# Performance work log

Measured on AMD Instinct MI355X. Metric: run time of the kernel, lower is better.

The kernel has to match this reference:

```python
import jax, jax.numpy as jnp
import numpy as np

B, N, E, DIN, DH = 32, 2000, 64000, 128, 128


def setup_inputs() -> dict:
    key = jax.random.key(0)
    ks = jax.random.split(key, 8)
    gene_emb = jax.random.normal(ks[0], (B, N, DIN), dtype=jnp.float32)
    edge_src = jax.random.randint(ks[1], (E,), 0, N, dtype=jnp.int32)
    edge_dst = jax.random.randint(ks[2], (E,), 0, N, dtype=jnp.int32)
    s1 = 1.0 / np.sqrt(DIN)
    s2 = 1.0 / np.sqrt(DH)
    W1 = jax.random.normal(ks[3], (DIN, DH), dtype=jnp.float32) * s1
    b1 = jnp.zeros((DH,), dtype=jnp.float32)
    W2 = jax.random.normal(ks[4], (DH, DH), dtype=jnp.float32) * s2
    b2 = jnp.zeros((DH,), dtype=jnp.float32)
    return {"gene_emb": gene_emb, "edge_src": edge_src, "edge_dst": edge_dst,
            "W1": W1, "b1": b1, "W2": W2, "b2": b2, "pathway_idx": 0}


def _gcn_conv(x, src, dst, norm_e, self_norm, W, b):
    # x: [B, N, Din] -> [B, N, Dout]; PyG GCNConv: linear first, then normalized aggregation
    h = jnp.einsum('bnd,de->bne', x, W)
    msgs = h[:, src, :] * norm_e[None, :, None]          # [B, E, Dout] gather
    agg = jax.vmap(lambda m: jax.ops.segment_sum(m, dst, num_segments=h.shape[1]))(msgs)
    # self-loop contribution (A+I): norm = dinv[i]^2
    return agg + h * self_norm[None, :, None] + b


def reference(gene_emb, edge_src, edge_dst, W1, b1, W2, b2, pathway_idx):
    n = gene_emb.shape[1]
    # symmetric GCN normalization with self loops: deg[i] = in_degree + 1
    deg = jnp.zeros((n,), dtype=gene_emb.dtype).at[edge_dst].add(1.0) + 1.0
    dinv = jax.lax.rsqrt(deg)
    norm_e = dinv[edge_src] * dinv[edge_dst]
    self_norm = dinv * dinv
    x = jax.nn.relu(_gcn_conv(gene_emb, edge_src, edge_dst, norm_e, self_norm, W1, b1))
    x = _gcn_conv(x, edge_src, edge_dst, norm_e, self_norm, W2, b2)
    # global_mean_pool over each graph copy (all graphs have n nodes)
    return jnp.mean(x, axis=1)  # [B, DH]
```

## Files before the change

kernel.cpp:

```cpp
#include <hip/hip_runtime.h>

namespace {
constexpr int NB = 32;
constexpr int NN = 2000;
constexpr int NE = 64000;
constexpr int ND = 128;
constexpr int TR = 16;
constexpr int NCHUNK = NN / TR;
constexpr int NXCD = 8;
constexpr int BPB = 2;
constexpr int PAIRS_PER_XCD = NB / (NXCD * BPB);
constexpr int NPAIR = NB / BPB;
constexpr int GRID_FUSED = NPAIR * NCHUNK;
constexpr int SL = 80;

constexpr int CVT_BLOCKS  = 1000;
constexpr int W_BLOCKS    = 8;
constexpr int EDGE_BLOCKS = 250;

constexpr size_t OFF_CNT    = 0;
constexpr size_t OFF_CNT2   = 8192;
constexpr size_t OFF_WSUM   = 16384;
constexpr size_t MEMSET_BYTES = 24576;
constexpr size_t OFF_SLOT2  = 24576;
constexpr size_t OFF_WF     = OFF_SLOT2 + (size_t)NN * SL * 8;
constexpr size_t OFF_YP     = OFF_WF + 32768;
constexpr size_t OFF_XBF    = OFF_YP + (size_t)NB * NCHUNK * ND * 4;

typedef __attribute__((ext_vector_type(8))) short bf16x8;
typedef __attribute__((ext_vector_type(4))) float f32x4;

__device__ __forceinline__ ushort f32_to_bf16(float f) {
    uint u = __float_as_uint(f);
    u += 0x7fffu + ((u >> 16) & 1u);
    return (ushort)(u >> 16);
}
__device__ __forceinline__ uint pack_bf16x2(float lo, float hi) {
    return (uint)f32_to_bf16(lo) | ((uint)f32_to_bf16(hi) << 16);
}
}

__global__ void k_prep1(const float* __restrict__ X, ushort* __restrict__ xbf,
                        const float* __restrict__ W1, uint* __restrict__ wf,
                        const int* __restrict__ dst, int* __restrict__ cnt) {
    const int blk = blockIdx.x;
    if (blk < CVT_BLOCKS) {
        const float4* __restrict__ X4 = (const float4*)X;
        ushort4* __restrict__ O4 = (ushort4*)xbf;
        const int base = blk * 2048 + (int)threadIdx.x;
        #pragma unroll
        for (int k = 0; k < 8; k++) {
            int i = base + k * 256;
            float4 v = X4[i];
            ushort4 o;
            o.x = f32_to_bf16(v.x);
            o.y = f32_to_bf16(v.y);
            o.z = f32_to_bf16(v.z);
            o.w = f32_to_bf16(v.w);
            O4[i] = o;
        }
    } else if (blk < CVT_BLOCKS + W_BLOCKS) {
        int g = (blk - CVT_BLOCKS) * 256 + threadIdx.x;
        int lane = g & 63, f = g >> 6;
        int nt = f >> 2, kc = f & 3;
        int col = nt * 16 + (lane & 15);
        int k0  = kc * 32 + (lane >> 4) * 8;
        uint4 o;
        o.x = pack_bf16x2(W1[(k0 + 0) * ND + col], W1[(k0 + 1) * ND + col]);
        o.y = pack_bf16x2(W1[(k0 + 2) * ND + col], W1[(k0 + 3) * ND + col]);
        o.z = pack_bf16x2(W1[(k0 + 4) * ND + col], W1[(k0 + 5) * ND + col]);
        o.w = pack_bf16x2(W1[(k0 + 6) * ND + col], W1[(k0 + 7) * ND + col]);
        ((uint4*)wf)[g] = o;
    } else {
        int e = (blk - CVT_BLOCKS - W_BLOCKS) * 256 + threadIdx.x;
        atomicAdd(&cnt[dst[e]], 1);
    }
}

__global__ void k_prep2(const int* __restrict__ src, const int* __restrict__ dst,
                        const int* __restrict__ cnt, int* __restrict__ cnt2,
                        float* __restrict__ wsum, int2* __restrict__ slot2) {
    int e = blockIdx.x * 256 + threadIdx.x;
    int s = src[e], d = dst[e];
    float w = rsqrtf((float)(cnt[s] + 1)) * rsqrtf((float)(cnt[d] + 1));
    int p = atomicAdd(&cnt2[d], 1);
    if (p < SL) slot2[(size_t)d * SL + p] = make_int2(s, __float_as_int(w));
    atomicAdd(&wsum[s], w);
}

__global__ __launch_bounds__(256, 4) void k_fused(const ushort* __restrict__ xbf,
                                                  const int* __restrict__ cnt,
                                                  const int2* __restrict__ slot2,
                                                  const float* __restrict__ wsum,
                                                  const uint* __restrict__ wfrag,
                                                  const float* __restrict__ b1,
                                                  float* __restrict__ ypart) {
    __shared__ __align__(16) uint AsU[2][TR * 68];
    __shared__ int2  sE[TR][SL];
    __shared__ float sDinv[TR];
    __shared__ float sWn[TR];
    __shared__ int   sCnt[TR];
    const int tid = threadIdx.x;

    const int L     = blockIdx.x;
    const int xcd   = L & (NXCD - 1);
    const int sl    = L >> 3;
    const int pair  = sl / NCHUNK;
    const int chunk = sl - pair * NCHUNK;
    const int b0    = xcd * (BPB * PAIRS_PER_XCD) + pair * BPB;
    const int n0    = chunk * TR;

    if (tid < TR) {
        int n = n0 + tid;
        int cr = cnt[n];
        float d = rsqrtf((float)(cr + 1));
        sCnt[tid]  = min(cr, SL);
        sDinv[tid] = d;
        sWn[tid]   = wsum[n] + d * d;
    }
    __syncthreads();

    const int wv = tid >> 6, ln = tid & 63;
    const int p = ln >> 5, col = ln & 31;
    const uint2* __restrict__ X0 = (const uint2*)(xbf + (size_t)b0 * NN * ND);
    const uint2* __restrict__ X1 = X0 + (size_t)NN * ND / 4;

    bf16x8 wfv[2][4];
    const bf16x8* Wf8 = (const bf16x8*)wfrag;
    #pragma unroll
    for (int nt2 = 0; nt2 < 2; nt2++)
        #pragma unroll
        for (int kc = 0; kc < 4; kc++)
            wfv[nt2][kc] = Wf8[(((2 * wv + nt2) * 4 + kc) * 64) + ln];

    #pragma unroll
    for (int ii = 0; ii < 4; ii++) {
        int j = wv * 4 + ii;
        int c = sCnt[j];
        const int2* sp = slot2 + (size_t)(n0 + j) * SL;
        for (int base = 0; base < c; base += 64)
            if (base + ln < c) sE[j][base + ln] = sp[base + ln];
    }

    #pragma unroll 1
    for (int ii = 0; ii < 4; ii++) {
        const int j = wv * 4 + ii;
        const int n = n0 + j;
        const int c = sCnt[j];
        float4 a  = {0.f, 0.f, 0.f, 0.f}, ab = a;
        float4 g  = a, gb = a;
        {
            uint2 q = X0[(size_t)p * (NN * ND / 4) + n * 32 + col];
            float sn = sDinv[j] * sDinv[j];
            float w0 = p ? 0.f : sn;
            float w1 = p ? sn : 0.f;
            float f0 = __uint_as_float(q.x << 16);
            float f1 = __uint_as_float(q.x & 0xffff0000u);
            float f2 = __uint_as_float(q.y << 16);
            float f3 = __uint_as_float(q.y & 0xffff0000u);
            a.x = w0 * f0; a.y = w0 * f1; a.z = w0 * f2; a.w = w0 * f3;
            g.x = w1 * f0; g.y = w1 * f1; g.z = w1 * f2; g.w = w1 * f3;
        }
        int e = 0;
        for (; e + 8 <= c; e += 8) {
            int sidx[4]; float w[4]; uint2 q0[4], q1[4];
            #pragma unroll
            for (int q = 0; q < 4; q++) {
                int2 ed = sE[j][e + 2 * q + p];
                sidx[q] = ed.x; w[q] = __int_as_float(ed.y);
            }
            #pragma unroll
            for (int q = 0; q < 4; q++) {
                int off = sidx[q] * 32 + col;
                q0[q] = X0[off];
                q1[q] = X1[off];
            }
            #pragma unroll
            for (int q = 0; q < 4; q++) {
                float f0 = __uint_as_float(q0[q].x << 16);
                float f1 = __uint_as_float(q0[q].x & 0xffff0000u);
                float f2 = __uint_as_float(q0[q].y << 16);
                float f3 = __uint_as_float(q0[q].y & 0xffff0000u);
                float h0 = __uint_as_float(q1[q].x << 16);
                float h1 = __uint_as_float(q1[q].x & 0xffff0000u);
                float h2 = __uint_as_float(q1[q].y << 16);
                float h3 = __uint_as_float(q1[q].y & 0xffff0000u);
                if (q & 1) {
                    ab.x = fmaf(w[q], f0, ab.x); ab.y = fmaf(w[q], f1, ab.y);
                    ab.z = fmaf(w[q], f2, ab.z); ab.w = fmaf(w[q], f3, ab.w);
                    gb.x = fmaf(w[q], h0, gb.x); gb.y = fmaf(w[q], h1, gb.y);
                    gb.z = fmaf(w[q], h2, gb.z); gb.w = fmaf(w[q], h3, gb.w);
                } else {
                    a.x = fmaf(w[q], f0, a.x); a.y = fmaf(w[q], f1, a.y);
                    a.z = fmaf(w[q], f2, a.z); a.w = fmaf(w[q], f3, a.w);
                    g.x = fmaf(w[q], h0, g.x); g.y = fmaf(w[q], h1, g.y);
                    g.z = fmaf(w[q], h2, g.z); g.w = fmaf(w[q], h3, g.w);
                }
            }
        }
        for (; e < c; e += 2) {
            int ee = e + p;
            int eidx = (ee < c) ? ee : e;
            int2 ed = sE[j][eidx];
            float w = (ee < c) ? __int_as_float(ed.y) : 0.f;
            int off = ed.x * 32 + col;
            uint2 u0 = X0[off], u1 = X1[off];
            a.x = fmaf(w, __uint_as_float(u0.x << 16), a.x);
            a.y = fmaf(w, __uint_as_float(u0.x & 0xffff0000u), a.y);
            a.z = fmaf(w, __uint_as_float(u0.y << 16), a.z);
            a.w = fmaf(w, __uint_as_float(u0.y & 0xffff0000u), a.w);
            g.x = fmaf(w, __uint_as_float(u1.x << 16), g.x);
            g.y = fmaf(w, __uint_as_float(u1.x & 0xffff0000u), g.y);
            g.z = fmaf(w, __uint_as_float(u1.y << 16), g.z);
            g.w = fmaf(w, __uint_as_float(u1.y & 0xffff0000u), g.w);
        }
        a.x += ab.x; a.y += ab.y; a.z += ab.z; a.w += ab.w;
        g.x += gb.x; g.y += gb.y; g.z += gb.z; g.w += gb.w;
        a.x += __shfl_xor(a.x, 32); a.y += __shfl_xor(a.y, 32);
        a.z += __shfl_xor(a.z, 32); a.w += __shfl_xor(a.w, 32);
        g.x += __shfl_xor(g.x, 32); g.y += __shfl_xor(g.y, 32);
        g.z += __shfl_xor(g.z, 32); g.w += __shfl_xor(g.w, 32);
        float4 av;
        av.x = p ? g.x : a.x; av.y = p ? g.y : a.y;
        av.z = p ? g.z : a.z; av.w = p ? g.w : a.w;
        AsU[p][j * 68 + 2 * col]     = pack_bf16x2(av.x, av.y);
        AsU[p][j * 68 + 2 * col + 1] = pack_bf16x2(av.z, av.w);
    }
    __syncthreads();

    const int lane15 = ln & 15, quad = ln >> 4;
    f32x4 zero4 = {0.f, 0.f, 0.f, 0.f};
    f32x4 acc[2][2];
    acc[0][0] = zero4; acc[0][1] = zero4; acc[1][0] = zero4; acc[1][1] = zero4;

    const bf16x8* A0 = (const bf16x8*)AsU[0];
    const bf16x8* A1 = (const bf16x8*)AsU[1];
    #pragma unroll
    for (int kc = 0; kc < 4; kc++) {
        bf16x8 af0 = A0[lane15 * 17 + kc * 4 + quad];
        bf16x8 af1 = A1[lane15 * 17 + kc * 4 + quad];
        #pragma unroll
        for (int nt2 = 0; nt2 < 2; nt2++) {
            acc[0][nt2] = __builtin_amdgcn_mfma_f32_16x16x32_bf16(
                af0, wfv[nt2][kc], acc[0][nt2], 0, 0, 0);
            acc[1][nt2] = __builtin_amdgcn_mfma_f32_16x16x32_bf16(
                af1, wfv[nt2][kc], acc[1][nt2], 0, 0, 0);
        }
    }

    #pragma unroll
    for (int nt2 = 0; nt2 < 2; nt2++) {
        int cg = (2 * wv + nt2) * 16 + lane15;
        float bias = b1[cg];
        #pragma unroll
        for (int b = 0; b < 2; b++) {
            float part = 0.f;
            #pragma unroll
            for (int r = 0; r < 4; r++)
                part = fmaf(sWn[quad * 4 + r], fmaxf(acc[b][nt2][r] + bias, 0.f), part);
            part += __shfl_xor(part, 16);
            part += __shfl_xor(part, 32);
            if (quad == 0)
                ypart[((size_t)(b0 + b) * NCHUNK + chunk) * ND + cg] = part;
        }
    }
}

__global__ __launch_bounds__(128) void k_out(const float* __restrict__ ypart,
                                             const float* __restrict__ W2,
                                             const float* __restrict__ b2,
                                             float* __restrict__ out) {
    __shared__ float ys[128];
    const int b = blockIdx.x;
    const int d = threadIdx.x;
    float s = 0.f;
    for (int c = 0; c < NCHUNK; c++)
        s += ypart[((size_t)b * NCHUNK + c) * ND + d];
    ys[d] = s * (1.f / (float)NN);
    __syncthreads();
    float acc = b2[d];
    #pragma unroll 8
    for (int k = 0; k < 128; k++)
        acc = fmaf(ys[k], W2[k * ND + d], acc);
    out[b * ND + d] = acc;
}

extern "C" void kernel_launch(void* const* d_in, const int* in_sizes, int n_in,
                              void* d_out, int out_size, void* d_ws, size_t ws_size,
                              hipStream_t stream) {
    (void)in_sizes; (void)n_in; (void)out_size; (void)ws_size;
    const float* X   = (const float*)d_in[0];
    const int*   src = (const int*)d_in[1];
    const int*   dst = (const int*)d_in[2];
    const float* W1  = (const float*)d_in[3];
    const float* b1  = (const float*)d_in[4];
    const float* W2  = (const float*)d_in[5];
    const float* b2  = (const float*)d_in[6];
    float* out = (float*)d_out;

    char* ws = (char*)d_ws;
    int*    cnt   = (int*)   (ws + OFF_CNT);
    int*    cnt2  = (int*)   (ws + OFF_CNT2);
    float*  wsum  = (float*) (ws + OFF_WSUM);
    int2*   slot2 = (int2*)  (ws + OFF_SLOT2);
    uint*   wfb   = (uint*)  (ws + OFF_WF);
    float*  ypart = (float*) (ws + OFF_YP);
    ushort* xbf   = (ushort*)(ws + OFF_XBF);

    (void)hipMemsetAsync(ws, 0, MEMSET_BYTES, stream);
    k_prep1<<<CVT_BLOCKS + W_BLOCKS + EDGE_BLOCKS, 256, 0, stream>>>(
        X, xbf, W1, wfb, dst, cnt);
    k_prep2<<<EDGE_BLOCKS, 256, 0, stream>>>(src, dst, cnt, cnt2, wsum, slot2);
    k_fused<<<GRID_FUSED, 256, 0, stream>>>(xbf, cnt, slot2, wsum, wfb, b1, ypart);
    k_out<<<NB, 128, 0, stream>>>(ypart, W2, b2, out);
}
```

Baseline: 169.0 us.

## Merge all stages into one cooperative persistent kernel with grid syncs

```diff
diff --git a/kernel.cpp b/kernel.cpp
--- a/kernel.cpp
+++ b/kernel.cpp
@@ -1,4 +1,7 @@
 #include <hip/hip_runtime.h>
+#include <hip/hip_cooperative_groups.h>
+
+namespace cg = cooperative_groups;
 
 namespace {
 constexpr int NB = 32;
@@ -10,10 +13,10 @@
 constexpr int NXCD = 8;
 constexpr int BPB = 2;
 constexpr int PAIRS_PER_XCD = NB / (NXCD * BPB);
-constexpr int NPAIR = NB / BPB;
-constexpr int GRID_FUSED = NPAIR * NCHUNK;
+constexpr int GRID_FUSED = (NB / BPB) * NCHUNK;
 constexpr int SL = 80;
 
+constexpr int GRID_MEGA   = 1000;
 constexpr int CVT_BLOCKS  = 1000;
 constexpr int W_BLOCKS    = 8;
 constexpr int EDGE_BLOCKS = 250;
@@ -38,6 +41,274 @@
 __device__ __forceinline__ uint pack_bf16x2(float lo, float hi) {
     return (uint)f32_to_bf16(lo) | ((uint)f32_to_bf16(hi) << 16);
 }
+
+__device__ __forceinline__ void wpack_item(const float* __restrict__ W1,
+                                           uint* __restrict__ wf, int g) {
+    int lane = g & 63, f = g >> 6;
+    int nt = f >> 2, kc = f & 3;
+    int colw = nt * 16 + (lane & 15);
+    int k0  = kc * 32 + (lane >> 4) * 8;
+    uint4 o;
+    o.x = pack_bf16x2(W1[(k0 + 0) * ND + colw], W1[(k0 + 1) * ND + colw]);
+    o.y = pack_bf16x2(W1[(k0 + 2) * ND + colw], W1[(k0 + 3) * ND + colw]);
+    o.z = pack_bf16x2(W1[(k0 + 4) * ND + colw], W1[(k0 + 5) * ND + colw]);
+    o.w = pack_bf16x2(W1[(k0 + 6) * ND + colw], W1[(k0 + 7) * ND + colw]);
+    ((uint4*)wf)[g] = o;
+}
+
+__device__ __forceinline__ void fused_tile(const ushort* __restrict__ xbf,
+                                           const int* __restrict__ cnt,
+                                           const int2* __restrict__ slot2,
+                                           const float* __restrict__ wsum,
+                                           const uint* __restrict__ wfrag,
+                                           const float* __restrict__ b1,
+                                           float* __restrict__ ypart,
+                                           int xcd, int chunk, int pair0, int npair,
+                                           int tid) {
+    __shared__ __align__(16) uint AsU[2][TR * 68];
+    __shared__ int2  sE[TR][SL];
+    __shared__ float sDinv[TR];
+    __shared__ float sWn[TR];
+    __shared__ int   sCnt[TR];
+
+    const int n0 = chunk * TR;
+    if (tid < TR) {
+        int n = n0 + tid;
+        int cr = cnt[n];
+        float d = rsqrtf((float)(cr + 1));
+        sCnt[tid]  = min(cr, SL);
+        sDinv[tid] = d;
+        sWn[tid]   = wsum[n] + d * d;
+    }
+    __syncthreads();
+
+    const int wv = tid >> 6, ln = tid & 63;
+    const int p = ln >> 5, col = ln & 31;
+
+    bf16x8 wfv[2][4];
+    const bf16x8* Wf8 = (const bf16x8*)wfrag;
+    #pragma unroll
+    for (int nt2 = 0; nt2 < 2; nt2++)
+        #pragma unroll
+        for (int kc = 0; kc < 4; kc++)
+            wfv[nt2][kc] = Wf8[(((2 * wv + nt2) * 4 + kc) * 64) + ln];
+
+    #pragma unroll
+    for (int ii = 0; ii < 4; ii++) {
+        int j = wv * 4 + ii;
+        int c = sCnt[j];
+        const int2* sp = slot2 + (size_t)(n0 + j) * SL;
+        for (int base = 0; base < c; base += 64)
+            if (base + ln < c) sE[j][base + ln] = sp[base + ln];
+    }
+
+    for (int pr = pair0; pr < pair0 + npair; ++pr) {
+        const int b0 = xcd * (BPB * PAIRS_PER_XCD) + pr * BPB;
+        const uint2* __restrict__ X0 = (const uint2*)(xbf + (size_t)b0 * NN * ND);
+        const uint2* __restrict__ X1 = X0 + (size_t)NN * ND / 4;
+
+        #pragma unroll 1
+        for (int ii = 0; ii < 4; ii++) {
+            const int j = wv * 4 + ii;
+            const int n = n0 + j;
+            const int c = sCnt[j];
+            float4 a  = {0.f, 0.f, 0.f, 0.f}, ab = a;
+            float4 g  = a, gb = a;
+            {
+                uint2 q = X0[(size_t)p * (NN * ND / 4) + n * 32 + col];
+                float sn = sDinv[j] * sDinv[j];
+                float w0 = p ? 0.f : sn;
+                float w1 = p ? sn : 0.f;
+                float f0 = __uint_as_float(q.x << 16);
+                float f1 = __uint_as_float(q.x & 0xffff0000u);
+                float f2 = __uint_as_float(q.y << 16);
+                float f3 = __uint_as_float(q.y & 0xffff0000u);
+                a.x = w0 * f0; a.y = w0 * f1; a.z = w0 * f2; a.w = w0 * f3;
+                g.x = w1 * f0; g.y = w1 * f1; g.z = w1 * f2; g.w = w1 * f3;
+            }
+            int e = 0;
+            for (; e + 8 <= c; e += 8) {
+                int sidx[4]; float w[4]; uint2 q0[4], q1[4];
+                #pragma unroll
+                for (int q = 0; q < 4; q++) {
+                    int2 ed = sE[j][e + 2 * q + p];
+                    sidx[q] = ed.x; w[q] = __int_as_float(ed.y);
+                }
+                #pragma unroll
+                for (int q = 0; q < 4; q++) {
+                    int off = sidx[q] * 32 + col;
+                    q0[q] = X0[off];
+                    q1[q] = X1[off];
+                }
+                #pragma unroll
+                for (int q = 0; q < 4; q++) {
+                    float f0 = __uint_as_float(q0[q].x << 16);
+                    float f1 = __uint_as_float(q0[q].x & 0xffff0000u);
+                    float f2 = __uint_as_float(q0[q].y << 16);
+                    float f3 = __uint_as_float(q0[q].y & 0xffff0000u);
+                    float h0 = __uint_as_float(q1[q].x << 16);
+                    float h1 = __uint_as_float(q1[q].x & 0xffff0000u);
+                    float h2 = __uint_as_float(q1[q].y << 16);
+                    float h3 = __uint_as_float(q1[q].y & 0xffff0000u);
+                    if (q & 1) {
+                        ab.x = fmaf(w[q], f0, ab.x); ab.y = fmaf(w[q], f1, ab.y);
+                        ab.z = fmaf(w[q], f2, ab.z); ab.w = fmaf(w[q], f3, ab.w);
+                        gb.x = fmaf(w[q], h0, gb.x); gb.y = fmaf(w[q], h1, gb.y);
+                        gb.z = fmaf(w[q], h2, gb.z); gb.w = fmaf(w[q], h3, gb.w);
+                    } else {
+                        a.x = fmaf(w[q], f0, a.x); a.y = fmaf(w[q], f1, a.y);
+                        a.z = fmaf(w[q], f2, a.z); a.w = fmaf(w[q], f3, a.w);
+                        g.x = fmaf(w[q], h0, g.x); g.y = fmaf(w[q], h1, g.y);
+                        g.z = fmaf(w[q], h2, g.z); g.w = fmaf(w[q], h3, g.w);
+                    }
+                }
+            }
+            for (; e < c; e += 2) {
+                int ee = e + p;
+                int eidx = (ee < c) ? ee : e;
+                int2 ed = sE[j][eidx];
+                float w = (ee < c) ? __int_as_float(ed.y) : 0.f;
+                int off = ed.x * 32 + col;
+                uint2 u0 = X0[off], u1 = X1[off];
+                a.x = fmaf(w, __uint_as_float(u0.x << 16), a.x);
+                a.y = fmaf(w, __uint_as_float(u0.x & 0xffff0000u), a.y);
+                a.z = fmaf(w, __uint_as_float(u0.y << 16), a.z);
+                a.w = fmaf(w, __uint_as_float(u0.y & 0xffff0000u), a.w);
+                g.x = fmaf(w, __uint_as_float(u1.x << 16), g.x);
+                g.y = fmaf(w, __uint_as_float(u1.x & 0xffff0000u), g.y);
+                g.z = fmaf(w, __uint_as_float(u1.y << 16), g.z);
+                g.w = fmaf(w, __uint_as_float(u1.y & 0xffff0000u), g.w);
+            }
+            a.x += ab.x; a.y += ab.y; a.z += ab.z; a.w += ab.w;
+            g.x += gb.x; g.y += gb.y; g.z += gb.z; g.w += gb.w;
+            a.x += __shfl_xor(a.x, 32); a.y += __shfl_xor(a.y, 32);
+            a.z += __shfl_xor(a.z, 32); a.w += __shfl_xor(a.w, 32);
+            g.x += __shfl_xor(g.x, 32); g.y += __shfl_xor(g.y, 32);
+            g.z += __shfl_xor(g.z, 32); g.w += __shfl_xor(g.w, 32);
+            float4 av;
+            av.x = p ? g.x : a.x; av.y = p ? g.y : a.y;
+            av.z = p ? g.z : a.z; av.w = p ? g.w : a.w;
+            AsU[p][j * 68 + 2 * col]     = pack_bf16x2(av.x, av.y);
+            AsU[p][j * 68 + 2 * col + 1] = pack_bf16x2(av.z, av.w);
+        }
+        __syncthreads();
+
+        const int lane15 = ln & 15, quad = ln >> 4;
+        f32x4 zero4 = {0.f, 0.f, 0.f, 0.f};
+        f32x4 acc[2][2];
+        acc[0][0] = zero4; acc[0][1] = zero4; acc[1][0] = zero4; acc[1][1] = zero4;
+
+        const bf16x8* A0 = (const bf16x8*)AsU[0];
+        const bf16x8* A1 = (const bf16x8*)AsU[1];
+        #pragma unroll
+        for (int kc = 0; kc < 4; kc++) {
+            bf16x8 af0 = A0[lane15 * 17 + kc * 4 + quad];
+            bf16x8 af1 = A1[lane15 * 17 + kc * 4 + quad];
+            #pragma unroll
+            for (int nt2 = 0; nt2 < 2; nt2++) {
+                acc[0][nt2] = __builtin_amdgcn_mfma_f32_16x16x32_bf16(
+                    af0, wfv[nt2][kc], acc[0][nt2], 0, 0, 0);
+                acc[1][nt2] = __builtin_amdgcn_mfma_f32_16x16x32_bf16(
+                    af1, wfv[nt2][kc], acc[1][nt2], 0, 0, 0);
+            }
+        }
+
+        #pragma unroll
+        for (int nt2 = 0; nt2 < 2; nt2++) {
+            int cg = (2 * wv + nt2) * 16 + lane15;
+            float bias = b1[cg];
+            #pragma unroll
+            for (int b = 0; b < 2; b++) {
+                float part = 0.f;
+                #pragma unroll
+                for (int r = 0; r < 4; r++)
+                    part = fmaf(sWn[quad * 4 + r], fmaxf(acc[b][nt2][r] + bias, 0.f),
+                                part);
+                part += __shfl_xor(part, 16);
+                part += __shfl_xor(part, 32);
+                if (quad == 0)
+                    ypart[((size_t)(b0 + b) * NCHUNK + chunk) * ND + cg] = part;
+            }
+        }
+        __syncthreads();
+    }
+}
+}
+
+__global__ __launch_bounds__(256, 4) void k_mega(const float* __restrict__ X,
+                                                 ushort* __restrict__ xbf,
+                                                 const float* __restrict__ W1,
+                                                 uint* __restrict__ wf,
+                                                 const int* __restrict__ src,
+                                                 const int* __restrict__ dst,
+                                                 int* __restrict__ cnt,
+                                                 int* __restrict__ cnt2,
+                                                 float* __restrict__ wsum,
+                                                 int2* __restrict__ slot2,
+                                                 const float* __restrict__ b1,
+                                                 float* __restrict__ ypart,
+                                                 const float* __restrict__ W2,
+                                                 const float* __restrict__ b2,
+                                                 float* __restrict__ out) {
+    cg::grid_group grid = cg::this_grid();
+    const int blk = blockIdx.x;
+    const int tid = threadIdx.x;
+
+    {
+        const float4* __restrict__ X4 = (const float4*)X;
+        ushort4* __restrict__ O4 = (ushort4*)xbf;
+        const int base = blk * 256 + tid;
+        #pragma unroll
+        for (int k = 0; k < 8; k++) {
+            int i = base + k * (GRID_MEGA * 256);
+            float4 v = X4[i];
+            ushort4 o;
+            o.x = f32_to_bf16(v.x);
+            o.y = f32_to_bf16(v.y);
+            o.z = f32_to_bf16(v.z);
+            o.w = f32_to_bf16(v.w);
+            O4[i] = o;
+        }
+        if (blk < EDGE_BLOCKS) {
+            int e = blk * 256 + tid;
+            atomicAdd(&cnt[dst[e]], 1);
+        } else if (blk < EDGE_BLOCKS + W_BLOCKS) {
+            wpack_item(W1, wf, (blk - EDGE_BLOCKS) * 256 + tid);
+        }
+    }
+    grid.sync();
+
+    if (blk < EDGE_BLOCKS) {
+        int e = blk * 256 + tid;
+        int s = src[e], d = dst[e];
+        float w = rsqrtf((float)(cnt[s] + 1)) * rsqrtf((float)(cnt[d] + 1));
+        int ps = atomicAdd(&cnt2[d], 1);
+        if (ps < SL) slot2[(size_t)d * SL + ps] = make_int2(s, __float_as_int(w));
+        atomicAdd(&wsum[s], w);
+    }
+    grid.sync();
+
+    fused_tile(xbf, cnt, slot2, wsum, wf, b1, ypart, blk & (NXCD - 1), blk >> 3,
+               0, PAIRS_PER_XCD, tid);
+    grid.sync();
+
+    if (blk < NB) {
+        __shared__ float ys[ND];
+        if (tid < ND) {
+            float s = 0.f;
+            for (int c = 0; c < NCHUNK; c++)
+                s += ypart[((size_t)blk * NCHUNK + c) * ND + tid];
+            ys[tid] = s * (1.f / (float)NN);
+        }
+        __syncthreads();
+        if (tid < ND) {
+            float a2 = b2[tid];
+            #pragma unroll 8
+            for (int k = 0; k < ND; k++)
+                a2 = fmaf(ys[k], W2[k * ND + tid], a2);
+            out[blk * ND + tid] = a2;
+        }
+    }
 }
 
 __global__ void k_prep1(const float* __restrict__ X, ushort* __restrict__ xbf,
@@ -60,17 +331,7 @@
             O4[i] = o;
         }
     } else if (blk < CVT_BLOCKS + W_BLOCKS) {
-        int g = (blk - CVT_BLOCKS) * 256 + threadIdx.x;
-        int lane = g & 63, f = g >> 6;
-        int nt = f >> 2, kc = f & 3;
-        int col = nt * 16 + (lane & 15);
-        int k0  = kc * 32 + (lane >> 4) * 8;
-        uint4 o;
-        o.x = pack_bf16x2(W1[(k0 + 0) * ND + col], W1[(k0 + 1) * ND + col]);
-        o.y = pack_bf16x2(W1[(k0 + 2) * ND + col], W1[(k0 + 3) * ND + col]);
-        o.z = pack_bf16x2(W1[(k0 + 4) * ND + col], W1[(k0 + 5) * ND + col]);
-        o.w = pack_bf16x2(W1[(k0 + 6) * ND + col], W1[(k0 + 7) * ND + col]);
-        ((uint4*)wf)[g] = o;
+        wpack_item(W1, wf, (blk - CVT_BLOCKS) * 256 + threadIdx.x);
     } else {
         int e = (blk - CVT_BLOCKS - W_BLOCKS) * 256 + threadIdx.x;
         atomicAdd(&cnt[dst[e]], 1);
@@ -83,8 +344,8 @@
     int e = blockIdx.x * 256 + threadIdx.x;
     int s = src[e], d = dst[e];
     float w = rsqrtf((float)(cnt[s] + 1)) * rsqrtf((float)(cnt[d] + 1));
-    int p = atomicAdd(&cnt2[d], 1);
-    if (p < SL) slot2[(size_t)d * SL + p] = make_int2(s, __float_as_int(w));
+    int ps = atomicAdd(&cnt2[d], 1);
+    if (ps < SL) slot2[(size_t)d * SL + ps] = make_int2(s, __float_as_int(w));
     atomicAdd(&wsum[s], w);
 }
 
@@ -95,175 +356,13 @@
                                                   const uint* __restrict__ wfrag,
                                                   const float* __restrict__ b1,
                                                   float* __restrict__ ypart) {
-    __shared__ __align__(16) uint AsU[2][TR * 68];
-    __shared__ int2  sE[TR][SL];
-    __shared__ float sDinv[TR];
-    __shared__ float sWn[TR];
-    __shared__ int   sCnt[TR];
-    const int tid = threadIdx.x;
-
     const int L     = blockIdx.x;
     const int xcd   = L & (NXCD - 1);
     const int sl    = L >> 3;
     const int pair  = sl / NCHUNK;
     const int chunk = sl - pair * NCHUNK;
-    const int b0    = xcd * (BPB * PAIRS_PER_XCD) + pair * BPB;
-    const int n0    = chunk * TR;
-
-    if (tid < TR) {
-        int n = n0 + tid;
-        int cr = cnt[n];
-        float d = rsqrtf((float)(cr + 1));
-        sCnt[tid]  = min(cr, SL);
-        sDinv[tid] = d;
-        sWn[tid]   = wsum[n] + d * d;
-    }
-    __syncthreads();
-
-    const int wv = tid >> 6, ln = tid & 63;
-    const int p = ln >> 5, col = ln & 31;
-    const uint2* __restrict__ X0 = (const uint2*)(xbf + (size_t)b0 * NN * ND);
-    const uint2* __restrict__ X1 = X0 + (size_t)NN * ND / 4;
-
-    bf16x8 wfv[2][4];
-    const bf16x8* Wf8 = (const bf16x8*)wfrag;
-    #pragma unroll
-    for (int nt2 = 0; nt2 < 2; nt2++)
-        #pragma unroll
-        for (int kc = 0; kc < 4; kc++)
-            wfv[nt2][kc] = Wf8[(((2 * wv + nt2) * 4 + kc) * 64) + ln];
-
-    #pragma unroll
-    for (int ii = 0; ii < 4; ii++) {
-        int j = wv * 4 + ii;
-        int c = sCnt[j];
-        const int2* sp = slot2 + (size_t)(n0 + j) * SL;
-        for (int base = 0; base < c; base += 64)
-            if (base + ln < c) sE[j][base + ln] = sp[base + ln];
-    }
-
-    #pragma unroll 1
-    for (int ii = 0; ii < 4; ii++) {
-        const int j = wv * 4 + ii;
-        const int n = n0 + j;
-        const int c = sCnt[j];
-        float4 a  = {0.f, 0.f, 0.f, 0.f}, ab = a;
-        float4 g  = a, gb = a;
-        {
-            uint2 q = X0[(size_t)p * (NN * ND / 4) + n * 32 + col];
-            float sn = sDinv[j] * sDinv[j];
-            float w0 = p ? 0.f : sn;
-            float w1 = p ? sn : 0.f;
-            float f0 = __uint_as_float(q.x << 16);
-            float f1 = __uint_as_float(q.x & 0xffff0000u);
-            float f2 = __uint_as_float(q.y << 16);
-            float f3 = __uint_as_float(q.y & 0xffff0000u);
-            a.x = w0 * f0; a.y = w0 * f1; a.z = w0 * f2; a.w = w0 * f3;
-            g.x = w1 * f0; g.y = w1 * f1; g.z = w1 * f2; g.w = w1 * f3;
-        }
-        int e = 0;
-        for (; e + 8 <= c; e += 8) {
-            int sidx[4]; float w[4]; uint2 q0[4], q1[4];
-            #pragma unroll
-            for (int q = 0; q < 4; q++) {
-                int2 ed = sE[j][e + 2 * q + p];
-                sidx[q] = ed.x; w[q] = __int_as_float(ed.y);
-            }
-            #pragma unroll
-            for (int q = 0; q < 4; q++) {
-                int off = sidx[q] * 32 + col;
-                q0[q] = X0[off];
-                q1[q] = X1[off];
-            }
-            #pragma unroll
-            for (int q = 0; q < 4; q++) {
-                float f0 = __uint_as_float(q0[q].x << 16);
-                float f1 = __uint_as_float(q0[q].x & 0xffff0000u);
-                float f2 = __uint_as_float(q0[q].y << 16);
-                float f3 = __uint_as_float(q0[q].y & 0xffff0000u);
-                float h0 = __uint_as_float(q1[q].x << 16);
-                float h1 = __uint_as_float(q1[q].x & 0xffff0000u);
-                float h2 = __uint_as_float(q1[q].y << 16);
-                float h3 = __uint_as_float(q1[q].y & 0xffff0000u);
-                if (q & 1) {
-                    ab.x = fmaf(w[q], f0, ab.x); ab.y = fmaf(w[q], f1, ab.y);
-                    ab.z = fmaf(w[q], f2, ab.z); ab.w = fmaf(w[q], f3, ab.w);
-                    gb.x = fmaf(w[q], h0, gb.x); gb.y = fmaf(w[q], h1, gb.y);
-                    gb.z = fmaf(w[q], h2, gb.z); gb.w = fmaf(w[q], h3, gb.w);
-                } else {
-                    a.x = fmaf(w[q], f0, a.x); a.y = fmaf(w[q], f1, a.y);
-                    a.z = fmaf(w[q], f2, a.z); a.w = fmaf(w[q], f3, a.w);
-                    g.x = fmaf(w[q], h0, g.x); g.y = fmaf(w[q], h1, g.y);
-                    g.z = fmaf(w[q], h2, g.z); g.w = fmaf(w[q], h3, g.w);
-                }
-            }
-        }
-        for (; e < c; e += 2) {
-            int ee = e + p;
-            int eidx = (ee < c) ? ee : e;
-            int2 ed = sE[j][eidx];
-            float w = (ee < c) ? __int_as_float(ed.y) : 0.f;
-            int off = ed.x * 32 + col;
-            uint2 u0 = X0[off], u1 = X1[off];
-            a.x = fmaf(w, __uint_as_float(u0.x << 16), a.x);
-            a.y = fmaf(w, __uint_as_float(u0.x & 0xffff0000u), a.y);
-            a.z = fmaf(w, __uint_as_float(u0.y << 16), a.z);
-            a.w = fmaf(w, __uint_as_float(u0.y & 0xffff0000u), a.w);
-            g.x = fmaf(w, __uint_as_float(u1.x << 16), g.x);
-            g.y = fmaf(w, __uint_as_float(u1.x & 0xffff0000u), g.y);
-            g.z = fmaf(w, __uint_as_float(u1.y << 16), g.z);
-            g.w = fmaf(w, __uint_as_float(u1.y & 0xffff0000u), g.w);
-        }
-        a.x += ab.x; a.y += ab.y; a.z += ab.z; a.w += ab.w;
-        g.x += gb.x; g.y += gb.y; g.z += gb.z; g.w += gb.w;
-        a.x += __shfl_xor(a.x, 32); a.y += __shfl_xor(a.y, 32);
-        a.z += __shfl_xor(a.z, 32); a.w += __shfl_xor(a.w, 32);
-        g.x += __shfl_xor(g.x, 32); g.y += __shfl_xor(g.y, 32);
-        g.z += __shfl_xor(g.z, 32); g.w += __shfl_xor(g.w, 32);
-        float4 av;
-        av.x = p ? g.x : a.x; av.y = p ? g.y : a.y;
-        av.z = p ? g.z : a.z; av.w = p ? g.w : a.w;
-        AsU[p][j * 68 + 2 * col]     = pack_bf16x2(av.x, av.y);
-        AsU[p][j * 68 + 2 * col + 1] = pack_bf16x2(av.z, av.w);
-    }
-    __syncthreads();
-
-    const int lane15 = ln & 15, quad = ln >> 4;
-    f32x4 zero4 = {0.f, 0.f, 0.f, 0.f};
-    f32x4 acc[2][2];
-    acc[0][0] = zero4; acc[0][1] = zero4; acc[1][0] = zero4; acc[1][1] = zero4;
-
-    const bf16x8* A0 = (const bf16x8*)AsU[0];
-    const bf16x8* A1 = (const bf16x8*)AsU[1];
-    #pragma unroll
-    for (int kc = 0; kc < 4; kc++) {
-        bf16x8 af0 = A0[lane15 * 17 + kc * 4 + quad];
-        bf16x8 af1 = A1[lane15 * 17 + kc * 4 + quad];
-        #pragma unroll
-        for (int nt2 = 0; nt2 < 2; nt2++) {
-            acc[0][nt2] = __builtin_amdgcn_mfma_f32_16x16x32_bf16(
-                af0, wfv[nt2][kc], acc[0][nt2], 0, 0, 0);
-            acc[1][nt2] = __builtin_amdgcn_mfma_f32_16x16x32_bf16(
-                af1, wfv[nt2][kc], acc[1][nt2], 0, 0, 0);
-        }
-    }
-
-    #pragma unroll
-    for (int nt2 = 0; nt2 < 2; nt2++) {
-        int cg = (2 * wv + nt2) * 16 + lane15;
-        float bias = b1[cg];
-        #pragma unroll
-        for (int b = 0; b < 2; b++) {
-            float part = 0.f;
-            #pragma unroll
-            for (int r = 0; r < 4; r++)
-                part = fmaf(sWn[quad * 4 + r], fmaxf(acc[b][nt2][r] + bias, 0.f), part);
-            part += __shfl_xor(part, 16);
-            part += __shfl_xor(part, 32);
-            if (quad == 0)
-                ypart[((size_t)(b0 + b) * NCHUNK + chunk) * ND + cg] = part;
-        }
-    }
+    fused_tile(xbf, cnt, slot2, wsum, wfrag, b1, ypart, xcd, chunk, pair, 1,
+               threadIdx.x);
 }
 
 __global__ __launch_bounds__(128) void k_out(const float* __restrict__ ypart,
@@ -308,9 +407,16 @@
     ushort* xbf   = (ushort*)(ws + OFF_XBF);
 
     (void)hipMemsetAsync(ws, 0, MEMSET_BYTES, stream);
-    k_prep1<<<CVT_BLOCKS + W_BLOCKS + EDGE_BLOCKS, 256, 0, stream>>>(
-        X, xbf, W1, wfb, dst, cnt);
-    k_prep2<<<EDGE_BLOCKS, 256, 0, stream>>>(src, dst, cnt, cnt2, wsum, slot2);
-    k_fused<<<GRID_FUSED, 256, 0, stream>>>(xbf, cnt, slot2, wsum, wfb, b1, ypart);
-    k_out<<<NB, 128, 0, stream>>>(ypart, W2, b2, out);
-}
+
+    void* args[] = {&X, &xbf, &W1, &wfb, &src, &dst, &cnt, &cnt2,
+                    &wsum, &slot2, &b1, &ypart, &W2, &b2, &out};
+    hipError_t cerr = hipLaunchCooperativeKernel(k_mega, dim3(GRID_MEGA), dim3(256),
+                                                 args, 0u, stream);
+    if (cerr != hipSuccess) {
+        k_prep1<<<CVT_BLOCKS + W_BLOCKS + EDGE_BLOCKS, 256, 0, stream>>>(
+            X, xbf, W1, wfb, dst, cnt);
+        k_prep2<<<EDGE_BLOCKS, 256, 0, stream>>>(src, dst, cnt, cnt2, wsum, slot2);
+        k_fused<<<GRID_FUSED, 256, 0, stream>>>(xbf, cnt, slot2, wsum, wfb, b1, ypart);
+        k_out<<<NB, 128, 0, stream>>>(ypart, W2, b2, out);
+    }
+}
```

New measurement: 519.5 us. +207.5%, slower.
